# Optimization experiments

Measured on AMD Instinct MI355X. Metric: run time of the kernel, lower is better.

The kernel has to match this reference:

```python
import jax, jax.numpy as jnp
import numpy as np

EPS = 1e-5
NHEAD = 8

def layer_norm(x, g, b):
    mu = jnp.mean(x, axis=-1, keepdims=True)
    var = jnp.mean((x - mu) ** 2, axis=-1, keepdims=True)
    return (x - mu) * jax.lax.rsqrt(var + EPS) * g + b

def setup_inputs() -> dict:
    key = jax.random.key(0)
    ks = jax.random.split(key, 8)
    B, S, D, F = 4, 2048, 512, 2048
    s = 0.02
    return {
        "x": jax.random.normal(ks[0], (B, S, D), jnp.float32),
        "Wqkv": jax.random.normal(ks[1], (3 * D, D), jnp.float32) * s,
        "bqkv": jnp.zeros((3 * D,), jnp.float32),
        "Wo": jax.random.normal(ks[2], (D, D), jnp.float32) * s,
        "bo": jnp.zeros((D,), jnp.float32),
        "W1": jax.random.normal(ks[3], (F, D), jnp.float32) * s,
        "b1": jnp.zeros((F,), jnp.float32),
        "W2": jax.random.normal(ks[4], (D, F), jnp.float32) * s,
        "b2": jnp.zeros((D,), jnp.float32),
        "g1": jnp.ones((D,), jnp.float32),
        "bn1": jnp.zeros((D,), jnp.float32),
        "g2": jnp.ones((D,), jnp.float32),
        "bn2": jnp.zeros((D,), jnp.float32),
    }

def reference(x, Wqkv, bqkv, Wo, bo, W1, b1, W2, b2, g1, bn1, g2, bn2):
    B, S, D = x.shape
    H = NHEAD
    hd = D // H
    # fused QKV projection (torch MultiheadAttention in_proj)
    qkv = x @ Wqkv.T + bqkv                      # [B,S,3D]
    q, k, v = jnp.split(qkv, 3, axis=-1)
    q = q.reshape(B, S, H, hd).transpose(0, 2, 1, 3)  # [B,H,S,hd]
    k = k.reshape(B, S, H, hd).transpose(0, 2, 1, 3)
    v = v.reshape(B, S, H, hd).transpose(0, 2, 1, 3)
    scores = jnp.einsum("bhqd,bhkd->bhqk", q, k) / jnp.sqrt(jnp.float32(hd))
    causal = jnp.tril(jnp.ones((S, S), bool))
    scores = jnp.where(causal, scores, jnp.float32(-jnp.inf))
    attn = jax.nn.softmax(scores, axis=-1)
    ctx = jnp.einsum("bhqk,bhkd->bhqd", attn, v)        # [B,H,S,hd]
    ctx = ctx.transpose(0, 2, 1, 3).reshape(B, S, D)
    attn_out = ctx @ Wo.T + bo
    # residual + LayerNorm 1
    x = layer_norm(x + attn_out, g1, bn1)
    # FFN (ReLU) + residual + LayerNorm 2
    ff = jax.nn.relu(x @ W1.T + b1) @ W2.T + b2
    x = layer_norm(x + ff, g2, bn2)
    return x
```

## Files before the change

### kernel.cpp

```cpp
#include <hip/hip_runtime.h>
#include <hip/hip_bf16.h>
#include <math.h>

#define D_MODEL 512
#define SEQ     2048
#define BATCH   4
#define NHEADS  8
#define HDIM    64
#define FFN     2048
#define TOKENS  (BATCH*SEQ)

typedef __attribute__((ext_vector_type(8))) short bf16x8;
typedef __attribute__((ext_vector_type(4))) float f32x4;
typedef __attribute__((ext_vector_type(4))) unsigned u32x4;

__device__ inline ushort f2bf(float f) {
    unsigned u = __builtin_bit_cast(unsigned, f);
    unsigned r = (u + 0x7fffu + ((u >> 16) & 1u)) >> 16;
    return (ushort)r;
}

#define GLOAD_LDS16(g, l) __builtin_amdgcn_global_load_lds( \
    (const __attribute__((address_space(1))) void*)(g), \
    (__attribute__((address_space(3))) void*)(l), 16, 0, 0)

__global__ void cast_all_bf16(const float* __restrict__ x, const float* __restrict__ Wqkv,
                              const float* __restrict__ Wo, const float* __restrict__ W1,
                              const float* __restrict__ W2, ushort* __restrict__ outbase) {
    const int i = blockIdx.x * blockDim.x + threadIdx.x;
    if (i >= 1835008) return;
    float4 v;
    if      (i < 1048576) v = ((const float4*)x)[i];
    else if (i < 1245184) v = ((const float4*)Wqkv)[i - 1048576];
    else if (i < 1310720) v = ((const float4*)Wo)[i - 1245184];
    else if (i < 1572864) v = ((const float4*)W1)[i - 1310720];
    else                  v = ((const float4*)W2)[i - 1572864];
    ushort4 o;
    o.x = f2bf(v.x); o.y = f2bf(v.y); o.z = f2bf(v.z); o.w = f2bf(v.w);
    ((ushort4*)outbase)[i] = o;
}

template<int MODE, int RELU, int BM>
__global__ __launch_bounds__(256) void gemm_bt_mfma(const ushort* __restrict__ A,
                                                    const ushort* __restrict__ W,
                                                    const float* __restrict__ bias,
                                                    void* __restrict__ CoutA,
                                                    ushort* __restrict__ Qc,
                                                    ushort* __restrict__ Kc,
                                                    ushort* __restrict__ Vt,
                                                    int M, int N, int Kstride, int Klen) {
    constexpr int MI = BM / 32;
    __shared__ ushort Asb[3][BM * 32];
    __shared__ ushort Bsb[3][128 * 32];

    const int tid  = threadIdx.x;
    const int lane = tid & 63;
    const int wv   = tid >> 6;

    const int Gx = gridDim.x;
    const int f  = blockIdx.x + Gx * blockIdx.y;
    const int xc = f & 7;
    const int j  = f >> 3;
    const int ni = j % Gx;
    const int mi = xc * (gridDim.y >> 3) + j / Gx;
    const int m0 = mi * BM;
    const int n0 = ni * 128;

    const int wm = (wv >> 1) * (BM / 2);
    const int wn = (wv & 1) * 64;

    const int rA = wv * (BM / 4) + (lane >> 2);
    const int rB = wv * 32 + (lane >> 2);
    const int cS = (((lane & 3) ^ ((lane >> 3) & 3)) * 8);
    const ushort* gA0 = A + (size_t)(m0 + rA) * Kstride + cS;
    const ushort* gA1 = gA0 + (size_t)16 * Kstride;
    const ushort* gB0 = W + (size_t)(n0 + rB) * Kstride + cS;
    const ushort* gB1 = gB0 + (size_t)16 * Kstride;

    f32x4 acc[MI][4] = {};

    const int fr  = lane & 15;
    const int fks = (((lane >> 4) ^ ((fr >> 1) & 3)) * 8);
    const int loA = wv * (BM * 32 / 4);
    const int loB = wv * 1024;

#define STAGE(ab, bb) do { \
        GLOAD_LDS16(gA0, (ab) + loA); \
        if constexpr (BM == 128) GLOAD_LDS16(gA1, (ab) + loA + 512); \
        GLOAD_LDS16(gB0, (bb) + loB); \
        GLOAD_LDS16(gB1, (bb) + loB + 512); \
        gA0 += 32; if constexpr (BM == 128) gA1 += 32; \
        gB0 += 32; gB1 += 32; } while (0)

#define COMPUTE(ab, bb) do { \
        bf16x8 af_[MI], bf_[4]; \
        _Pragma("unroll") \
        for (int i_ = 0; i_ < MI; ++i_) \
            af_[i_] = *(const bf16x8*)((ab) + (wm + i_ * 16 + fr) * 32 + fks); \
        _Pragma("unroll") \
        for (int j_ = 0; j_ < 4; ++j_) \
            bf_[j_] = *(const bf16x8*)((bb) + (wn + j_ * 16 + fr) * 32 + fks); \
        _Pragma("unroll") \
        for (int i_ = 0; i_ < MI; ++i_) \
            _Pragma("unroll") \
            for (int j_ = 0; j_ < 4; ++j_) \
                acc[i_][j_] = __builtin_amdgcn_mfma_f32_16x16x32_bf16(af_[i_], bf_[j_], acc[i_][j_], 0, 0, 0); \
        } while (0)

#define PWAIT do { \
        if constexpr (BM == 128) asm volatile("s_waitcnt vmcnt(4)" ::: "memory"); \
        else                     asm volatile("s_waitcnt vmcnt(3)" ::: "memory"); \
        __builtin_amdgcn_s_barrier(); \
        __builtin_amdgcn_sched_barrier(0); } while (0)

    ushort *Ac = Asb[0], *An = Asb[1], *As = Asb[2];
    ushort *Bc = Bsb[0], *Bn = Bsb[1], *Bs = Bsb[2];

    STAGE(Ac, Bc);
    STAGE(An, Bn);
    const int ntiles = Klen >> 5;
    for (int t = 0; t < ntiles - 1; ++t) {
        PWAIT;
        if (t + 2 < ntiles) STAGE(As, Bs);
        COMPUTE(Ac, Bc);
        ushort* tA = Ac; Ac = An; An = As; As = tA;
        ushort* tB = Bc; Bc = Bn; Bn = Bs; Bs = tB;
    }
    asm volatile("s_waitcnt vmcnt(0)" ::: "memory");
    __builtin_amdgcn_s_barrier();
    __builtin_amdgcn_sched_barrier(0);
    COMPUTE(Ac, Bc);

#undef STAGE
#undef COMPUTE
#undef PWAIT

    const int col  = lane & 15;
    const int rowq = (lane >> 4) * 4;
    #pragma unroll
    for (int i = 0; i < MI; ++i) {
        const int gm = m0 + wm + i * 16 + rowq;
        #pragma unroll
        for (int j2 = 0; j2 < 4; ++j2) {
            const int gn = n0 + wn + j2 * 16 + col;
            if (MODE == 2) {
                const float bv = bias[gn];
                const int seg = gn >> 9;
                const int h   = (gn >> 6) & 7;
                const int dd  = gn & 63;
                const int bb  = gm >> 11;
                const int ss  = gm & 2047;
                const int bh  = bb * 8 + h;
                if (seg == 2) {
                    ushort4 pk;
                    pk.x = f2bf(acc[i][j2][0] + bv);
                    pk.y = f2bf(acc[i][j2][1] + bv);
                    pk.z = f2bf(acc[i][j2][2] + bv);
                    pk.w = f2bf(acc[i][j2][3] + bv);
                    *(ushort4*)(Vt + ((size_t)bh * 64 + dd) * 2048 + ss) = pk;
                } else {
                    ushort* dst = (seg == 0 ? Qc : Kc) + ((size_t)bh * 2048 + ss) * 64 + dd;
                    #pragma unroll
                    for (int r = 0; r < 4; ++r)
                        dst[(size_t)r * 64] = f2bf(acc[i][j2][r] + bv);
                }
            } else if (MODE == 3) {
                float* dst = (float*)CoutA;
                const float bv = bias[gn];
                #pragma unroll
                for (int r = 0; r < 4; ++r)
                    dst[(size_t)(gm + r) * N + gn] = acc[i][j2][r] + bv;
            } else {
                const float bv = bias[gn];
                #pragma unroll
                for (int r = 0; r < 4; ++r) {
                    float v = acc[i][j2][r] + bv;
                    if (RELU) v = fmaxf(v, 0.f);
                    ((ushort*)CoutA)[(size_t)(gm + r) * N + gn] = f2bf(v);
                }
            }
        }
    }
}

__device__ __forceinline__ void attn_step(const ushort* __restrict__ Kb,
                                          const ushort* __restrict__ Vb,
                                          bf16x8 qf0, bf16x8 qf1,
                                          float& lp, f32x4 (&o)[4],
                                          int qw, int j0, bool diag,
                                          int col, int g, int c7) {
    f32x4 s[4] = {};
    __builtin_amdgcn_s_setprio(1);
    #pragma unroll
    for (int nt = 0; nt < 4; ++nt) {
        const int kr = nt * 16 + col;
        bf16x8 kf0 = *(const bf16x8*)(Kb + kr * 64 + (((g    ) ^ c7) * 8));
        bf16x8 kf1 = *(const bf16x8*)(Kb + kr * 64 + (((g + 4) ^ c7) * 8));
        s[nt] = __builtin_amdgcn_mfma_f32_16x16x32_bf16(kf0, qf0, s[nt], 0, 0, 0);
        s[nt] = __builtin_amdgcn_mfma_f32_16x16x32_bf16(kf1, qf1, s[nt], 0, 0, 0);
    }
    __builtin_amdgcn_s_setprio(0);

    if (diag) {
        #pragma unroll
        for (int nt = 0; nt < 4; ++nt)
            #pragma unroll
            for (int r = 0; r < 4; ++r)
                if ((j0 + nt * 16 + 4 * g + r) > (qw + col)) s[nt][r] = -INFINITY;
    }

    unsigned W[8];
    #pragma unroll
    for (int nt = 0; nt < 4; ++nt) {
        float p0 = __expf(s[nt][0] * 0.125f);
        float p1 = __expf(s[nt][1] * 0.125f);
        float p2 = __expf(s[nt][2] * 0.125f);
        float p3 = __expf(s[nt][3] * 0.125f);
        lp += (p0 + p1) + (p2 + p3);
        asm("v_cvt_pk_bf16_f32 %0, %1, %2" : "=v"(W[2 * nt])     : "v"(p0), "v"(p1));
        asm("v_cvt_pk_bf16_f32 %0, %1, %2" : "=v"(W[2 * nt + 1]) : "v"(p2), "v"(p3));
    }
    asm("v_permlane32_swap_b32 %0, %1" : "+v"(W[0]), "+v"(W[2]));
    asm("v_permlane32_swap_b32 %0, %1" : "+v"(W[1]), "+v"(W[3]));
    asm("v_permlane32_swap_b32 %0, %1" : "+v"(W[4]), "+v"(W[6]));
    asm("v_permlane32_swap_b32 %0, %1" : "+v"(W[5]), "+v"(W[7]));
    asm("v_permlane16_swap_b32 %0, %1" : "+v"(W[0]), "+v"(W[2]));
    asm("v_permlane16_swap_b32 %0, %1" : "+v"(W[1]), "+v"(W[3]));
    asm("v_permlane16_swap_b32 %0, %1" : "+v"(W[4]), "+v"(W[6]));
    asm("v_permlane16_swap_b32 %0, %1" : "+v"(W[5]), "+v"(W[7]));

    u32x4 wa = {W[0], W[1], W[2], W[3]};
    u32x4 wb = {W[4], W[5], W[6], W[7]};
    bf16x8 pf0 = __builtin_bit_cast(bf16x8, wa);
    bf16x8 pf1 = __builtin_bit_cast(bf16x8, wb);

    __builtin_amdgcn_s_setprio(1);
    #pragma unroll
    for (int nt = 0; nt < 4; ++nt) {
        const int vr = nt * 16 + col;
        bf16x8 vf0 = *(const bf16x8*)(Vb + vr * 64 + (((g    ) ^ c7) * 8));
        bf16x8 vf1 = *(const bf16x8*)(Vb + vr * 64 + (((g + 4) ^ c7) * 8));
        o[nt] = __builtin_amdgcn_mfma_f32_16x16x32_bf16(pf0, vf0, o[nt], 0, 0, 0);
        o[nt] = __builtin_amdgcn_mfma_f32_16x16x32_bf16(pf1, vf1, o[nt], 0, 0, 0);
    }
    __builtin_amdgcn_s_setprio(0);
}

__global__ __launch_bounds__(256, 4) void attn_mfma_kernel(const ushort* __restrict__ Qc,
                                                           const ushort* __restrict__ Kc,
                                                           const ushort* __restrict__ Vt,
                                                           ushort* __restrict__ ctxb) {
    __shared__ ushort Ks[2 * 64 * 64];
    __shared__ ushort Vs[2 * 64 * 64];

    const int tid  = threadIdx.x;
    const int lane = tid & 63;
    const int wv   = tid >> 6;
    const int idx  = blockIdx.x;
    const int bh   = (idx & 7) * 4 + (idx >> 7);
    const int pair = (idx >> 3) & 15;
    const int q0a  = pair * 64;
    const int q0b  = (31 - pair) * 64;
    const int qwA  = q0a + wv * 16;
    const int qwB  = q0b + wv * 16;

    const int col = lane & 15;
    const int g   = lane >> 4;
    const int c7  = col & 7;

    bf16x8 qfA0, qfA1, qfB0, qfB1;
    {
        const ushort* qa = Qc + ((size_t)bh * 2048 + qwA + col) * 64 + g * 8;
        qfA0 = *(const bf16x8*)qa;
        qfA1 = *(const bf16x8*)(qa + 32);
        const ushort* qb = Qc + ((size_t)bh * 2048 + qwB + col) * 64 + g * 8;
        qfB0 = *(const bf16x8*)qb;
        qfB1 = *(const bf16x8*)(qb + 32);
    }

    const int srow = tid >> 2;
    const int sch  = 2 * (tid & 3);
    const ushort* Kg = Kc + ((size_t)bh * 2048 + srow) * 64 + sch * 8;
    const ushort* Vg = Vt + ((size_t)bh * 64 + srow) * 2048 + sch * 8;
    const int ko0 = srow * 64 + (((sch    ) ^ (srow & 7)) * 8);
    const int ko1 = srow * 64 + (((sch + 1) ^ (srow & 7)) * 8);

    float lpa = 0.f, lpb = 0.f;
    f32x4 oa[4] = {}, ob[4] = {};

    bf16x8 pk0 = *(const bf16x8*)(Kg);
    bf16x8 pk1 = *(const bf16x8*)(Kg + 8);
    bf16x8 pv0 = *(const bf16x8*)(Vg);
    bf16x8 pv1 = *(const bf16x8*)(Vg + 8);

    for (int j0 = 0; j0 <= q0b; j0 += 64) {
        const int par = (j0 >> 6) & 1;
        ushort* Kb = Ks + par * 4096;
        ushort* Vb = Vs + par * 4096;
        *(bf16x8*)(Kb + ko0) = pk0; *(bf16x8*)(Kb + ko1) = pk1;
        *(bf16x8*)(Vb + ko0) = pv0; *(bf16x8*)(Vb + ko1) = pv1;
        __syncthreads();

        if (j0 < q0b) {
            pk0 = *(const bf16x8*)(Kg + (size_t)(j0 + 64) * 64);
            pk1 = *(const bf16x8*)(Kg + (size_t)(j0 + 64) * 64 + 8);
            pv0 = *(const bf16x8*)(Vg + j0 + 64);
            pv1 = *(const bf16x8*)(Vg + j0 + 72);
        }

        if (j0 <= q0a)
            attn_step(Kb, Vb, qfA0, qfA1, lpa, oa, qwA, j0, j0 == q0a, col, g, c7);
        attn_step(Kb, Vb, qfB0, qfB1, lpb, ob, qwB, j0, j0 == q0b, col, g, c7);
    }

    float la = lpa; la += __shfl_xor(la, 16); la += __shfl_xor(la, 32);
    float lb = lpb; lb += __shfl_xor(lb, 16); lb += __shfl_xor(lb, 32);
    const int b = bh >> 3, h = bh & 7;
    #pragma unroll
    for (int r = 0; r < 4; ++r) {
        const float inva = 1.f / __shfl(la, 4 * g + r);
        const float invb = 1.f / __shfl(lb, 4 * g + r);
        const size_t rowa = ((size_t)b * 2048 + qwA + 4 * g + r) * 512 + h * 64;
        const size_t rowb = ((size_t)b * 2048 + qwB + 4 * g + r) * 512 + h * 64;
        #pragma unroll
        for (int nt = 0; nt < 4; ++nt) {
            ctxb[rowa + nt * 16 + col] = f2bf(oa[nt][r] * inva);
            ctxb[rowb + nt * 16 + col] = f2bf(ob[nt][r] * invb);
        }
    }
}

template<int WRITE_BF16>
__global__ void ln_residual(const float* __restrict__ A, const float* __restrict__ B1,
                            const float* __restrict__ g, const float* __restrict__ beta,
                            float* __restrict__ out, ushort* __restrict__ outb) {
    __shared__ float sbuf[8];
    const int row = blockIdx.x;
    const int tid = threadIdx.x;
    const size_t base = (size_t)row * D_MODEL;

    float v0 = A[base + tid]       + B1[base + tid];
    float v1 = A[base + tid + 256] + B1[base + tid + 256];

    float sum = v0 + v1;
    #pragma unroll
    for (int off = 32; off; off >>= 1) sum += __shfl_xor(sum, off);
    if ((tid & 63) == 0) sbuf[tid >> 6] = sum;
    __syncthreads();
    if (tid == 0) { float t = 0.f; for (int i = 0; i < 4; ++i) t += sbuf[i]; sbuf[4] = t; }
    __syncthreads();
    const float mu = sbuf[4] * (1.f / 512.f);
    __syncthreads();

    float d0 = v0 - mu, d1 = v1 - mu;
    float sq = d0 * d0 + d1 * d1;
    #pragma unroll
    for (int off = 32; off; off >>= 1) sq += __shfl_xor(sq, off);
    if ((tid & 63) == 0) sbuf[tid >> 6] = sq;
    __syncthreads();
    if (tid == 0) { float t = 0.f; for (int i = 0; i < 4; ++i) t += sbuf[i]; sbuf[4] = t; }
    __syncthreads();
    const float var = sbuf[4] * (1.f / 512.f);
    const float rs  = rsqrtf(var + 1e-5f);

    float r0 = d0 * rs * g[tid]       + beta[tid];
    float r1 = d1 * rs * g[tid + 256] + beta[tid + 256];
    out[base + tid]       = r0;
    out[base + tid + 256] = r1;
    if (WRITE_BF16) {
        outb[base + tid]       = f2bf(r0);
        outb[base + tid + 256] = f2bf(r1);
    }
}

extern "C" void kernel_launch(void* const* d_in, const int* in_sizes, int n_in,
                              void* d_out, int out_size, void* d_ws, size_t ws_size,
                              hipStream_t stream) {
    const float* x    = (const float*)d_in[0];
    const float* Wqkv = (const float*)d_in[1];
    const float* bqkv = (const float*)d_in[2];
    const float* Wo   = (const float*)d_in[3];
    const float* bo   = (const float*)d_in[4];
    const float* W1   = (const float*)d_in[5];
    const float* b1   = (const float*)d_in[6];
    const float* W2   = (const float*)d_in[7];
    const float* b2   = (const float*)d_in[8];
    const float* g1   = (const float*)d_in[9];
    const float* bn1  = (const float*)d_in[10];
    const float* g2   = (const float*)d_in[11];
    const float* bn2  = (const float*)d_in[12];

    float* ws = (float*)d_ws;
    ushort* Qcb     = (ushort*)ws;
    ushort* Kcb     = (ushort*)(ws + 2097152);
    ushort* Vtb     = (ushort*)(ws + 4194304);
    ushort* ff1b    = (ushort*)ws;
    float*  ff2a    = ws + 8388608;
    float*  attn_a  = ws + 12582912;
    float*  ln1     = ws + 16777216;
    ushort* ctxb  = (ushort*)(ws + 20971520);
    ushort* ln1b  = (ushort*)(ws + 23068672);
    ushort* xb    = (ushort*)(ws + 25165824);
    ushort* Wqkvb = (ushort*)(ws + 27262976);
    float*  out   = (float*)d_out;
    ushort* W1b   = (ushort*)(ws + 27787264);
    ushort* W2b   = (ushort*)(ws + 28311552);
    ushort* Wob   = (ushort*)(ws + 27656192);

    const dim3 blk(256);

    cast_all_bf16<<<dim3(7168), blk, 0, stream>>>(x, Wqkv, Wo, W1, W2, xb);

    gemm_bt_mfma<2,0,128><<<dim3(1536/128, 8192/128), blk, 0, stream>>>(
        xb, Wqkvb, bqkv, nullptr, Qcb, Kcb, Vtb, TOKENS, 1536, 512, 512);
    attn_mfma_kernel<<<dim3(512), blk, 0, stream>>>(Qcb, Kcb, Vtb, ctxb);
    gemm_bt_mfma<3,0,64><<<dim3(512/128, 8192/64), blk, 0, stream>>>(
        ctxb, Wob, bo, attn_a, nullptr, nullptr, nullptr, TOKENS, 512, 512, 512);
    ln_residual<1><<<dim3(TOKENS), blk, 0, stream>>>(x, attn_a, g1, bn1, ln1, ln1b);
    gemm_bt_mfma<1,1,64><<<dim3(2048/128, 8192/64), blk, 0, stream>>>(
        ln1b, W1b, b1, ff1b, nullptr, nullptr, nullptr, TOKENS, 2048, 512, 512);
    gemm_bt_mfma<3,0,64><<<dim3(512/128, 8192/64), blk, 0, stream>>>(
        ff1b, W2b, b2, ff2a, nullptr, nullptr, nullptr, TOKENS, 512, 2048, 2048);
    ln_residual<0><<<dim3(TOKENS), blk, 0, stream>>>(ln1, ff2a, g2, bn2, out, nullptr);
}
```

Before: 247.6 us.

## Split paired causal query tiles into one tile per block, longest first

```diff
diff --git a/kernel.cpp b/kernel.cpp
--- a/kernel.cpp
+++ b/kernel.cpp
@@ -257,25 +257,21 @@
     const int lane = tid & 63;
     const int wv   = tid >> 6;
     const int idx  = blockIdx.x;
-    const int bh   = (idx & 7) * 4 + (idx >> 7);
-    const int pair = (idx >> 3) & 15;
-    const int q0a  = pair * 64;
-    const int q0b  = (31 - pair) * 64;
-    const int qwA  = q0a + wv * 16;
-    const int qwB  = q0b + wv * 16;
+    const int slot = idx >> 3;
+    const int bh   = (idx & 7) * 4 + (slot & 3);
+    const int qt   = 31 - (slot >> 2);
+    const int q0   = qt * 64;
+    const int qw   = q0 + wv * 16;
 
     const int col = lane & 15;
     const int g   = lane >> 4;
     const int c7  = col & 7;
 
-    bf16x8 qfA0, qfA1, qfB0, qfB1;
+    bf16x8 qf0, qf1;
     {
-        const ushort* qa = Qc + ((size_t)bh * 2048 + qwA + col) * 64 + g * 8;
-        qfA0 = *(const bf16x8*)qa;
-        qfA1 = *(const bf16x8*)(qa + 32);
-        const ushort* qb = Qc + ((size_t)bh * 2048 + qwB + col) * 64 + g * 8;
-        qfB0 = *(const bf16x8*)qb;
-        qfB1 = *(const bf16x8*)(qb + 32);
+        const ushort* qa = Qc + ((size_t)bh * 2048 + qw + col) * 64 + g * 8;
+        qf0 = *(const bf16x8*)qa;
+        qf1 = *(const bf16x8*)(qa + 32);
     }
 
     const int srow = tid >> 2;
@@ -285,15 +281,15 @@
     const int ko0 = srow * 64 + (((sch    ) ^ (srow & 7)) * 8);
     const int ko1 = srow * 64 + (((sch + 1) ^ (srow & 7)) * 8);
 
-    float lpa = 0.f, lpb = 0.f;
-    f32x4 oa[4] = {}, ob[4] = {};
+    float lp = 0.f;
+    f32x4 o[4] = {};
 
     bf16x8 pk0 = *(const bf16x8*)(Kg);
     bf16x8 pk1 = *(const bf16x8*)(Kg + 8);
     bf16x8 pv0 = *(const bf16x8*)(Vg);
     bf16x8 pv1 = *(const bf16x8*)(Vg + 8);
 
-    for (int j0 = 0; j0 <= q0b; j0 += 64) {
+    for (int j0 = 0; j0 <= q0; j0 += 64) {
         const int par = (j0 >> 6) & 1;
         ushort* Kb = Ks + par * 4096;
         ushort* Vb = Vs + par * 4096;
@@ -301,32 +297,25 @@
         *(bf16x8*)(Vb + ko0) = pv0; *(bf16x8*)(Vb + ko1) = pv1;
         __syncthreads();
 
-        if (j0 < q0b) {
+        if (j0 < q0) {
             pk0 = *(const bf16x8*)(Kg + (size_t)(j0 + 64) * 64);
             pk1 = *(const bf16x8*)(Kg + (size_t)(j0 + 64) * 64 + 8);
             pv0 = *(const bf16x8*)(Vg + j0 + 64);
             pv1 = *(const bf16x8*)(Vg + j0 + 72);
         }
 
-        if (j0 <= q0a)
-            attn_step(Kb, Vb, qfA0, qfA1, lpa, oa, qwA, j0, j0 == q0a, col, g, c7);
-        attn_step(Kb, Vb, qfB0, qfB1, lpb, ob, qwB, j0, j0 == q0b, col, g, c7);
-    }
-
-    float la = lpa; la += __shfl_xor(la, 16); la += __shfl_xor(la, 32);
-    float lb = lpb; lb += __shfl_xor(lb, 16); lb += __shfl_xor(lb, 32);
+        attn_step(Kb, Vb, qf0, qf1, lp, o, qw, j0, j0 == q0, col, g, c7);
+    }
+
+    float la = lp; la += __shfl_xor(la, 16); la += __shfl_xor(la, 32);
     const int b = bh >> 3, h = bh & 7;
     #pragma unroll
     for (int r = 0; r < 4; ++r) {
         const float inva = 1.f / __shfl(la, 4 * g + r);
-        const float invb = 1.f / __shfl(lb, 4 * g + r);
-        const size_t rowa = ((size_t)b * 2048 + qwA + 4 * g + r) * 512 + h * 64;
-        const size_t rowb = ((size_t)b * 2048 + qwB + 4 * g + r) * 512 + h * 64;
+        const size_t rowa = ((size_t)b * 2048 + qw + 4 * g + r) * 512 + h * 64;
         #pragma unroll
-        for (int nt = 0; nt < 4; ++nt) {
-            ctxb[rowa + nt * 16 + col] = f2bf(oa[nt][r] * inva);
-            ctxb[rowb + nt * 16 + col] = f2bf(ob[nt][r] * invb);
-        }
+        for (int nt = 0; nt < 4; ++nt)
+            ctxb[rowa + nt * 16 + col] = f2bf(o[nt][r] * inva);
     }
 }
 
@@ -413,7 +402,7 @@
 
     gemm_bt_mfma<2,0,128><<<dim3(1536/128, 8192/128), blk, 0, stream>>>(
         xb, Wqkvb, bqkv, nullptr, Qcb, Kcb, Vtb, TOKENS, 1536, 512, 512);
-    attn_mfma_kernel<<<dim3(512), blk, 0, stream>>>(Qcb, Kcb, Vtb, ctxb);
+    attn_mfma_kernel<<<dim3(1024), blk, 0, stream>>>(Qcb, Kcb, Vtb, ctxb);
     gemm_bt_mfma<3,0,64><<<dim3(512/128, 8192/64), blk, 0, stream>>>(
         ctxb, Wob, bo, attn_a, nullptr, nullptr, nullptr, TOKENS, 512, 512, 512);
     ln_residual<1><<<dim3(TOKENS), blk, 0, stream>>>(x, attn_a, g1, bn1, ln1, ln1b);
```

New measurement: 248.0 us. About the same (+0.2%).

## Double attention KV tile to 128 and use 128x256 tiles for FFN1 GEMM

Applied to the files above, without the earlier changes.

```diff
diff --git a/kernel.cpp b/kernel.cpp
--- a/kernel.cpp
+++ b/kernel.cpp
@@ -40,18 +40,23 @@
     ((ushort4*)outbase)[i] = o;
 }
 
-template<int MODE, int RELU, int BM>
-__global__ __launch_bounds__(256) void gemm_bt_mfma(const ushort* __restrict__ A,
-                                                    const ushort* __restrict__ W,
-                                                    const float* __restrict__ bias,
-                                                    void* __restrict__ CoutA,
-                                                    ushort* __restrict__ Qc,
-                                                    ushort* __restrict__ Kc,
-                                                    ushort* __restrict__ Vt,
-                                                    int M, int N, int Kstride, int Klen) {
-    constexpr int MI = BM / 32;
+template<int MODE, int RELU, int BM, int BN>
+__global__ __launch_bounds__(BN == 256 ? 512 : 256)
+void gemm_bt_mfma(const ushort* __restrict__ A,
+                  const ushort* __restrict__ W,
+                  const float* __restrict__ bias,
+                  void* __restrict__ CoutA,
+                  ushort* __restrict__ Qc,
+                  ushort* __restrict__ Kc,
+                  ushort* __restrict__ Vt,
+                  int M, int N, int Kstride, int Klen) {
+    constexpr int NW    = (BN == 256) ? 8 : 4;
+    constexpr int WC    = NW / 2;
+    constexpr int MI    = BM / 32;
+    constexpr int AROWS = BM / NW;
+    constexpr bool A2   = (AROWS == 32);
     __shared__ ushort Asb[3][BM * 32];
-    __shared__ ushort Bsb[3][128 * 32];
+    __shared__ ushort Bsb[3][BN * 32];
 
     const int tid  = threadIdx.x;
     const int lane = tid & 63;
@@ -64,12 +69,12 @@
     const int ni = j % Gx;
     const int mi = xc * (gridDim.y >> 3) + j / Gx;
     const int m0 = mi * BM;
-    const int n0 = ni * 128;
-
-    const int wm = (wv >> 1) * (BM / 2);
-    const int wn = (wv & 1) * 64;
-
-    const int rA = wv * (BM / 4) + (lane >> 2);
+    const int n0 = ni * BN;
+
+    const int wm = (wv / WC) * (BM / 2);
+    const int wn = (wv % WC) * 64;
+
+    const int rA = wv * AROWS + (lane >> 2);
     const int rB = wv * 32 + (lane >> 2);
     const int cS = (((lane & 3) ^ ((lane >> 3) & 3)) * 8);
     const ushort* gA0 = A + (size_t)(m0 + rA) * Kstride + cS;
@@ -81,15 +86,15 @@
 
     const int fr  = lane & 15;
     const int fks = (((lane >> 4) ^ ((fr >> 1) & 3)) * 8);
-    const int loA = wv * (BM * 32 / 4);
+    const int loA = wv * (AROWS * 32);
     const int loB = wv * 1024;
 
 #define STAGE(ab, bb) do { \
         GLOAD_LDS16(gA0, (ab) + loA); \
-        if constexpr (BM == 128) GLOAD_LDS16(gA1, (ab) + loA + 512); \
+        if constexpr (A2) GLOAD_LDS16(gA1, (ab) + loA + 512); \
         GLOAD_LDS16(gB0, (bb) + loB); \
         GLOAD_LDS16(gB1, (bb) + loB + 512); \
-        gA0 += 32; if constexpr (BM == 128) gA1 += 32; \
+        gA0 += 32; if constexpr (A2) gA1 += 32; \
         gB0 += 32; gB1 += 32; } while (0)
 
 #define COMPUTE(ab, bb) do { \
@@ -108,8 +113,8 @@
         } while (0)
 
 #define PWAIT do { \
-        if constexpr (BM == 128) asm volatile("s_waitcnt vmcnt(4)" ::: "memory"); \
-        else                     asm volatile("s_waitcnt vmcnt(3)" ::: "memory"); \
+        if constexpr (A2) asm volatile("s_waitcnt vmcnt(4)" ::: "memory"); \
+        else              asm volatile("s_waitcnt vmcnt(3)" ::: "memory"); \
         __builtin_amdgcn_s_barrier(); \
         __builtin_amdgcn_sched_barrier(0); } while (0)
 
@@ -184,7 +189,7 @@
 }
 
 __device__ __forceinline__ void attn_step(const ushort* __restrict__ Kb,
-                                          const ushort* __restrict__ Vb,
+                                          const ushort* __restrict__ Vb, int soff,
                                           bf16x8 qf0, bf16x8 qf1,
                                           float& lp, f32x4 (&o)[4],
                                           int qw, int j0, bool diag,
@@ -238,8 +243,8 @@
     #pragma unroll
     for (int nt = 0; nt < 4; ++nt) {
         const int vr = nt * 16 + col;
-        bf16x8 vf0 = *(const bf16x8*)(Vb + vr * 64 + (((g    ) ^ c7) * 8));
-        bf16x8 vf1 = *(const bf16x8*)(Vb + vr * 64 + (((g + 4) ^ c7) * 8));
+        bf16x8 vf0 = *(const bf16x8*)(Vb + vr * 128 + soff + (((g    ) ^ c7) * 8));
+        bf16x8 vf1 = *(const bf16x8*)(Vb + vr * 128 + soff + (((g + 4) ^ c7) * 8));
         o[nt] = __builtin_amdgcn_mfma_f32_16x16x32_bf16(pf0, vf0, o[nt], 0, 0, 0);
         o[nt] = __builtin_amdgcn_mfma_f32_16x16x32_bf16(pf1, vf1, o[nt], 0, 0, 0);
     }
@@ -250,8 +255,8 @@
                                                            const ushort* __restrict__ Kc,
                                                            const ushort* __restrict__ Vt,
                                                            ushort* __restrict__ ctxb) {
-    __shared__ ushort Ks[2 * 64 * 64];
-    __shared__ ushort Vs[2 * 64 * 64];
+    __shared__ ushort Ks[2 * 128 * 64];
+    __shared__ ushort Vs[2 * 64 * 128];
 
     const int tid  = threadIdx.x;
     const int lane = tid & 63;
@@ -280,37 +285,56 @@
 
     const int srow = tid >> 2;
     const int sch  = 2 * (tid & 3);
-    const ushort* Kg = Kc + ((size_t)bh * 2048 + srow) * 64 + sch * 8;
-    const ushort* Vg = Vt + ((size_t)bh * 64 + srow) * 2048 + sch * 8;
-    const int ko0 = srow * 64 + (((sch    ) ^ (srow & 7)) * 8);
-    const int ko1 = srow * 64 + (((sch + 1) ^ (srow & 7)) * 8);
+    const ushort* Kg  = Kc + ((size_t)bh * 2048 + srow) * 64 + sch * 8;
+    const ushort* Kg2 = Kg + 64 * 64;
+    const ushort* Vg  = Vt + ((size_t)bh * 64 + srow) * 2048 + sch * 8;
+    const int ko0 = srow * 64  + (((sch    ) ^ (srow & 7)) * 8);
+    const int ko1 = srow * 64  + (((sch + 1) ^ (srow & 7)) * 8);
+    const int vo0 = srow * 128 + (((sch    ) ^ (srow & 7)) * 8);
+    const int vo1 = srow * 128 + (((sch + 1) ^ (srow & 7)) * 8);
 
     float lpa = 0.f, lpb = 0.f;
     f32x4 oa[4] = {}, ob[4] = {};
 
     bf16x8 pk0 = *(const bf16x8*)(Kg);
     bf16x8 pk1 = *(const bf16x8*)(Kg + 8);
+    bf16x8 pk2 = *(const bf16x8*)(Kg2);
+    bf16x8 pk3 = *(const bf16x8*)(Kg2 + 8);
     bf16x8 pv0 = *(const bf16x8*)(Vg);
     bf16x8 pv1 = *(const bf16x8*)(Vg + 8);
-
-    for (int j0 = 0; j0 <= q0b; j0 += 64) {
-        const int par = (j0 >> 6) & 1;
-        ushort* Kb = Ks + par * 4096;
-        ushort* Vb = Vs + par * 4096;
+    bf16x8 pv2 = *(const bf16x8*)(Vg + 64);
+    bf16x8 pv3 = *(const bf16x8*)(Vg + 72);
+
+    for (int jt = 0; jt <= q0b; jt += 128) {
+        const int par = (jt >> 7) & 1;
+        ushort* Kb = Ks + par * 8192;
+        ushort* Vb = Vs + par * 8192;
         *(bf16x8*)(Kb + ko0) = pk0; *(bf16x8*)(Kb + ko1) = pk1;
-        *(bf16x8*)(Vb + ko0) = pv0; *(bf16x8*)(Vb + ko1) = pv1;
+        *(bf16x8*)(Kb + ko0 + 4096) = pk2; *(bf16x8*)(Kb + ko1 + 4096) = pk3;
+        *(bf16x8*)(Vb + vo0) = pv0; *(bf16x8*)(Vb + vo1) = pv1;
+        *(bf16x8*)(Vb + vo0 + 64) = pv2; *(bf16x8*)(Vb + vo1 + 64) = pv3;
         __syncthreads();
 
-        if (j0 < q0b) {
-            pk0 = *(const bf16x8*)(Kg + (size_t)(j0 + 64) * 64);
-            pk1 = *(const bf16x8*)(Kg + (size_t)(j0 + 64) * 64 + 8);
-            pv0 = *(const bf16x8*)(Vg + j0 + 64);
-            pv1 = *(const bf16x8*)(Vg + j0 + 72);
+        if (jt + 128 <= q0b) {
+            const size_t kb = (size_t)(jt + 128) * 64;
+            pk0 = *(const bf16x8*)(Kg + kb);
+            pk1 = *(const bf16x8*)(Kg + kb + 8);
+            pk2 = *(const bf16x8*)(Kg2 + kb);
+            pk3 = *(const bf16x8*)(Kg2 + kb + 8);
+            pv0 = *(const bf16x8*)(Vg + jt + 128);
+            pv1 = *(const bf16x8*)(Vg + jt + 136);
+            pv2 = *(const bf16x8*)(Vg + jt + 192);
+            pv3 = *(const bf16x8*)(Vg + jt + 200);
         }
 
-        if (j0 <= q0a)
-            attn_step(Kb, Vb, qfA0, qfA1, lpa, oa, qwA, j0, j0 == q0a, col, g, c7);
-        attn_step(Kb, Vb, qfB0, qfB1, lpb, ob, qwB, j0, j0 == q0b, col, g, c7);
+        if (jt <= q0a)
+            attn_step(Kb, Vb, 0, qfA0, qfA1, lpa, oa, qwA, jt, jt == q0a, col, g, c7);
+        attn_step(Kb, Vb, 0, qfB0, qfB1, lpb, ob, qwB, jt, jt == q0b, col, g, c7);
+        const int j1 = jt + 64;
+        if (j1 <= q0a)
+            attn_step(Kb + 4096, Vb, 64, qfA0, qfA1, lpa, oa, qwA, j1, j1 == q0a, col, g, c7);
+        if (j1 <= q0b)
+            attn_step(Kb + 4096, Vb, 64, qfB0, qfB1, lpb, ob, qwB, j1, j1 == q0b, col, g, c7);
     }
 
     float la = lpa; la += __shfl_xor(la, 16); la += __shfl_xor(la, 32);
@@ -411,15 +435,15 @@
 
     cast_all_bf16<<<dim3(7168), blk, 0, stream>>>(x, Wqkv, Wo, W1, W2, xb);
 
-    gemm_bt_mfma<2,0,128><<<dim3(1536/128, 8192/128), blk, 0, stream>>>(
+    gemm_bt_mfma<2,0,128,128><<<dim3(1536/128, 8192/128), blk, 0, stream>>>(
         xb, Wqkvb, bqkv, nullptr, Qcb, Kcb, Vtb, TOKENS, 1536, 512, 512);
     attn_mfma_kernel<<<dim3(512), blk, 0, stream>>>(Qcb, Kcb, Vtb, ctxb);
-    gemm_bt_mfma<3,0,64><<<dim3(512/128, 8192/64), blk, 0, stream>>>(
+    gemm_bt_mfma<3,0,64,128><<<dim3(512/128, 8192/64), blk, 0, stream>>>(
         ctxb, Wob, bo, attn_a, nullptr, nullptr, nullptr, TOKENS, 512, 512, 512);
     ln_residual<1><<<dim3(TOKENS), blk, 0, stream>>>(x, attn_a, g1, bn1, ln1, ln1b);
-    gemm_bt_mfma<1,1,64><<<dim3(2048/128, 8192/64), blk, 0, stream>>>(
+    gemm_bt_mfma<1,1,128,256><<<dim3(2048/256, 8192/128), dim3(512), 0, stream>>>(
         ln1b, W1b, b1, ff1b, nullptr, nullptr, nullptr, TOKENS, 2048, 512, 512);
-    gemm_bt_mfma<3,0,64><<<dim3(512/128, 8192/64), blk, 0, stream>>>(
+    gemm_bt_mfma<3,0,64,128><<<dim3(512/128, 8192/64), blk, 0, stream>>>(
         ff1b, W2b, b2, ff2a, nullptr, nullptr, nullptr, TOKENS, 512, 2048, 2048);
     ln_residual<0><<<dim3(TOKENS), blk, 0, stream>>>(ln1, ff2a, g2, bn2, out, nullptr);
 }
```

Result: no change. 248.2 us (+0.3%).
